# Kernel optimization log

Hardware: AMD Instinct MI355X
Metric: run time of the kernel (lower is better)

Reference implementation:

```python
import jax, jax.numpy as jnp
import numpy as np

B, NPG, DEG, F, H, C = 256, 256, 16, 128, 128, 10
N = B * NPG
E = N * DEG
RATIO = 0.5
K1 = int(np.ceil(RATIO * NPG))       # 128
K2 = int(np.ceil(RATIO * K1))        # 64
K3 = int(np.ceil(RATIO * K2))        # 32


def _glorot(key, shape):
    lim = np.sqrt(6.0 / (shape[0] + shape[1]))
    return jax.random.uniform(key, shape, jnp.float32, -lim, lim)


def setup_inputs() -> dict:
    key = jax.random.key(0)
    ks = jax.random.split(key, 16)
    x = jax.random.normal(ks[0], (N, F), jnp.float32)
    epg = E // B
    g = jnp.repeat(jnp.arange(B, dtype=jnp.int32), epg)
    src = jax.random.randint(ks[1], (E,), 0, NPG, jnp.int32) + g * NPG
    dst = jax.random.randint(ks[2], (E,), 0, NPG, jnp.int32) + g * NPG
    edge_index = jnp.stack([src, dst])
    batch = jnp.repeat(jnp.arange(B, dtype=jnp.int32), NPG)
    return {
        "x": x, "edge_index": edge_index, "batch": batch,
        "W1": _glorot(ks[3], (F, H)), "b1": jnp.zeros((H,), jnp.float32),
        "Wp1": _glorot(ks[4], (H, 1)), "bp1": jnp.zeros((1,), jnp.float32),
        "W2": _glorot(ks[5], (H, H)), "b2": jnp.zeros((H,), jnp.float32),
        "Wp2": _glorot(ks[6], (H, 1)), "bp2": jnp.zeros((1,), jnp.float32),
        "W3": _glorot(ks[7], (H, H)), "b3": jnp.zeros((H,), jnp.float32),
        "Wp3": _glorot(ks[8], (H, 1)), "bp3": jnp.zeros((1,), jnp.float32),
        "Wl1": _glorot(ks[9], (2 * H, H)), "bl1": jnp.zeros((H,), jnp.float32),
        "Wl2": _glorot(ks[10], (H, H // 2)), "bl2": jnp.zeros((H // 2,), jnp.float32),
        "Wl3": _glorot(ks[11], (H // 2, C)), "bl3": jnp.zeros((C,), jnp.float32),
    }


def gcn_conv(x, src, dst, emask, nmask, W, b):
    # PyG GCNConv: symmetric normalization with self-loops, edge weights = emask.
    h = x @ W
    deg = jax.ops.segment_sum(emask, dst, num_segments=N) + nmask  # self-loop on active nodes
    dinv = jnp.where(deg > 0, jax.lax.rsqrt(deg), 0.0)
    w = emask * dinv[src] * dinv[dst]                      # [E]
    agg = jax.ops.segment_sum(h[src] * w[:, None], dst, num_segments=N)
    out = agg + h * (dinv * dinv * nmask)[:, None] + b
    return out * nmask[:, None]


def topk_pool(x, src, dst, emask, nmask, Wp, bp, k):
    # SAGPool-style gcn_pool: score via GCNConv(H->1), per-graph top-k,
    # x <- x * tanh(score) on kept nodes, edges restricted to kept nodes.
    s = gcn_conv(x, src, dst, emask, nmask, Wp, bp)[:, 0]   # [N]
    sm = jnp.where(nmask > 0, s, -jnp.inf).reshape(B, NPG)
    idx = jax.lax.top_k(sm, k)[1]                           # [B,k]
    newmask = jnp.zeros((B, NPG), x.dtype).at[jnp.arange(B)[:, None], idx].set(1.0).reshape(-1)
    x_new = x * jnp.tanh(s)[:, None] * newmask[:, None]
    emask_new = emask * newmask[src] * newmask[dst]
    return x_new, emask_new, newmask


def readout(x, nmask, batch):
    # cat([global_max_pool, global_mean_pool]) over remaining nodes per graph
    cnt = jax.ops.segment_sum(nmask, batch, num_segments=B)
    mean = jax.ops.segment_sum(x, batch, num_segments=B) / cnt[:, None]
    xinf = jnp.where(nmask[:, None] > 0, x, -jnp.inf)
    mx = jax.ops.segment_max(xinf, batch, num_segments=B)
    return jnp.concatenate([mx, mean], axis=1)


def reference(x, edge_index, batch, W1, b1, Wp1, bp1, W2, b2, Wp2, bp2, W3, b3, Wp3, bp3,
              Wl1, bl1, Wl2, bl2, Wl3, bl3):
    src, dst = edge_index[0], edge_index[1]
    emask = jnp.ones((E,), x.dtype)
    nmask = jnp.ones((N,), x.dtype)

    h = jax.nn.relu(gcn_conv(x, src, dst, emask, nmask, W1, b1))
    h, emask, nmask = topk_pool(h, src, dst, emask, nmask, Wp1, bp1, K1)
    x1 = readout(h, nmask, batch)

    h = jax.nn.relu(gcn_conv(h, src, dst, emask, nmask, W2, b2))
    h, emask, nmask = topk_pool(h, src, dst, emask, nmask, Wp2, bp2, K2)
    x2 = readout(h, nmask, batch)

    h = jax.nn.relu(gcn_conv(h, src, dst, emask, nmask, W3, b3))
    h, emask, nmask = topk_pool(h, src, dst, emask, nmask, Wp3, bp3, K3)
    x3 = readout(h, nmask, batch)

    z = x1 + x2 + x3
    z = jax.nn.relu(z @ Wl1 + bl1)   # dropout is identity in eval mode
    z = jax.nn.relu(z @ Wl2 + bl2)
    return jax.nn.log_softmax(z @ Wl3 + bl3, axis=-1)
```

## Files before the change

### kernel.cpp

```cpp
#include <hip/hip_runtime.h>
#include <math.h>

#define NB   256
#define NPG  256
#define NN   (NB * NPG)
#define NE   (NN * 16)
#define EPG  (NE / NB)
#define FD   128
#define NC   10
#define NSL  32
#define NEG_INF (-3.402823466e38f)

struct SM {
    float hs[NPG][FD];
    int   rp[NPG + 4];
    float nmloc[NPG];
    float dvv[NPG];
    float sw[NPG];
    float sf[NPG];
    float svv[NPG];
    float th[NPG];
    float zacc[2 * FD];
    int   si[NPG];
    int   kept[NPG];
    int   anode[NPG];
    float red_mx[16][FD];
    float red_sm[16][FD];
    unsigned char colb[EPG];
};

__device__ __forceinline__ float4& hsq(SM& sm, int v, int q) {
    return *(float4*)&sm.hs[v][(q ^ (v & 7)) << 2];
}

template <int NACT>
__device__ __forceinline__ void do_level(SM& sm,
                                         const float* __restrict__ Wmat,
                                         const float* __restrict__ bias,
                                         const float* __restrict__ Wp,
                                         const float* __restrict__ bpp,
                                         int tid) {
    constexpr int NPS = NACT / NSL;
    constexpr int K   = NACT / 2;
    constexpr int TPN = 1024 / NACT;
    const int f4 = tid & 31;
    const int s  = tid >> 5;

    {
        const int n = tid >> 2, sub = tid & 3;
        float part = 0.f;
        const float nmn = sm.nmloc[n];
        if (nmn > 0.f) {
            const int e1 = sm.rp[n + 1];
            for (int e = sm.rp[n] + sub; e < e1; e += 4)
                part += sm.nmloc[sm.colb[e]];
        }
        part += __shfl_xor(part, 1);
        part += __shfl_xor(part, 2);
        if (sub == 0)
            sm.dvv[n] = (nmn > 0.f) ? rsqrtf(1.f + part) : 0.f;
    }

    {
        int vr[NPS];
        float4 acc[NPS];
#pragma unroll
        for (int c = 0; c < NPS; ++c) {
            vr[c] = sm.anode[c * NSL + s];
            acc[c] = make_float4(0.f, 0.f, 0.f, 0.f);
        }
#pragma unroll 2
        for (int kq = 0; kq < 32; ++kq) {
            const int k0 = kq << 2;
            float4 w0 = *(const float4*)&Wmat[(k0 + 0) * FD + 4 * f4];
            float4 w1 = *(const float4*)&Wmat[(k0 + 1) * FD + 4 * f4];
            float4 w2 = *(const float4*)&Wmat[(k0 + 2) * FD + 4 * f4];
            float4 w3 = *(const float4*)&Wmat[(k0 + 3) * FD + 4 * f4];
#pragma unroll
            for (int c = 0; c < NPS; ++c) {
                float4 hv = hsq(sm, vr[c], kq);
                acc[c].x += hv.x * w0.x + hv.y * w1.x + hv.z * w2.x + hv.w * w3.x;
                acc[c].y += hv.x * w0.y + hv.y * w1.y + hv.z * w2.y + hv.w * w3.y;
                acc[c].z += hv.x * w0.z + hv.y * w1.z + hv.z * w2.z + hv.w * w3.z;
                acc[c].w += hv.x * w0.w + hv.y * w1.w + hv.z * w2.w + hv.w * w3.w;
            }
        }
#pragma unroll
        for (int c = 0; c < NPS; ++c)
            hsq(sm, vr[c], f4) = acc[c];
    }
    __syncthreads();

    const float4 b4  = *(const float4*)&bias[4 * f4];
    const float4 wp4 = *(const float4*)&Wp[4 * f4];
    float4 hreg[NPS];
#pragma unroll
    for (int c = 0; c < NPS; ++c) {
        const int v = sm.anode[c * NSL + s];
        const float dv_ = sm.dvv[v], dv2 = dv_ * dv_;
        const float4 hv = hsq(sm, v, f4);
        float4 acc;
        acc.x = hv.x * dv2 + b4.x;
        acc.y = hv.y * dv2 + b4.y;
        acc.z = hv.z * dv2 + b4.z;
        acc.w = hv.w * dv2 + b4.w;
        const int e0 = sm.rp[v], e1 = sm.rp[v + 1];
        int e = e0;
        for (; e + 4 <= e1; e += 4) {
            int u0 = sm.colb[e],     u1 = sm.colb[e + 1];
            int u2 = sm.colb[e + 2], u3 = sm.colb[e + 3];
            float w0 = sm.dvv[u0] * dv_, w1 = sm.dvv[u1] * dv_;
            float w2 = sm.dvv[u2] * dv_, w3 = sm.dvv[u3] * dv_;
            float4 h0 = hsq(sm, u0, f4);
            float4 h1 = hsq(sm, u1, f4);
            float4 h2 = hsq(sm, u2, f4);
            float4 h3 = hsq(sm, u3, f4);
            acc.x += w0 * h0.x + w1 * h1.x + w2 * h2.x + w3 * h3.x;
            acc.y += w0 * h0.y + w1 * h1.y + w2 * h2.y + w3 * h3.y;
            acc.z += w0 * h0.z + w1 * h1.z + w2 * h2.z + w3 * h3.z;
            acc.w += w0 * h0.w + w1 * h1.w + w2 * h2.w + w3 * h3.w;
        }
        for (; e < e1; ++e) {
            int u = sm.colb[e];
            float w = sm.dvv[u] * dv_;
            float4 hu = hsq(sm, u, f4);
            acc.x += w * hu.x; acc.y += w * hu.y;
            acc.z += w * hu.z; acc.w += w * hu.w;
        }
        acc.x = fmaxf(acc.x, 0.f);
        acc.y = fmaxf(acc.y, 0.f);
        acc.z = fmaxf(acc.z, 0.f);
        acc.w = fmaxf(acc.w, 0.f);
        hreg[c] = acc;
        float p = acc.x * wp4.x + acc.y * wp4.y + acc.z * wp4.z + acc.w * wp4.w;
        p += __shfl_xor(p, 1);
        p += __shfl_xor(p, 2);
        p += __shfl_xor(p, 4);
        p += __shfl_xor(p, 8);
        p += __shfl_xor(p, 16);
        if (f4 == 0) sm.sw[v] = p;
    }
    __syncthreads();

    {
        const int i = tid / TPN, sub = tid % TPN;
        const int v = sm.anode[i];
        const float dv_ = sm.dvv[v];
        float part = 0.f;
        const int e1 = sm.rp[v + 1];
        for (int e = sm.rp[v] + sub; e < e1; e += TPN) {
            int u = sm.colb[e];
            part += sm.dvv[u] * sm.sw[u];
        }
#pragma unroll
        for (int o = 1; o < TPN; o <<= 1) part += __shfl_xor(part, o);
        if (sub == 0) {
            float acc = sm.sw[v] * dv_ * dv_ + bpp[0] + dv_ * part;
            sm.sf[v] = acc;
            sm.svv[i] = acc;
        }
    }
    __syncthreads();

    float v_ = 0.f;
    int   id_ = 0;
    if (tid < NACT) { v_ = sm.svv[tid]; id_ = sm.anode[tid]; }
#pragma unroll
    for (int k = 2; k <= NACT; k <<= 1) {
#pragma unroll
        for (int j = k >> 1; j > 0; j >>= 1) {
            if (j < 64) {
                if (tid < NACT) {
                    float vp = __shfl_xor(v_, j);
                    int  idp = __shfl_xor(id_, j);
                    bool up    = ((tid & k) == 0);
                    bool lower = ((tid & j) == 0);
                    bool g = (v_ > vp) || (v_ == vp && id_ < idp);
                    if (g != (lower == up)) { v_ = vp; id_ = idp; }
                }
            } else {
                if (tid < NACT) { sm.svv[tid] = v_; sm.si[tid] = id_; }
                __syncthreads();
                if (tid < NACT) {
                    int p = tid ^ j;
                    float vp = sm.svv[p];
                    int  idp = sm.si[p];
                    bool up    = ((tid & k) == 0);
                    bool lower = ((tid & j) == 0);
                    bool g = (v_ > vp) || (v_ == vp && id_ < idp);
                    if (g != (lower == up)) { v_ = vp; id_ = idp; }
                }
                __syncthreads();
            }
        }
    }
    if (tid < NPG) sm.kept[tid] = 0;
    __syncthreads();
    if (tid < K) {
        sm.kept[id_] = 1;
        sm.th[id_] = tanhf(sm.sf[id_]);
    }
    __syncthreads();

    float4 mx4 = make_float4(NEG_INF, NEG_INF, NEG_INF, NEG_INF);
    float4 sm4 = make_float4(0.f, 0.f, 0.f, 0.f);
#pragma unroll
    for (int c = 0; c < NPS; ++c) {
        const int v = sm.anode[c * NSL + s];
        if (sm.kept[v]) {
            const float tg = sm.th[v];
            float4 val;
            val.x = hreg[c].x * tg;
            val.y = hreg[c].y * tg;
            val.z = hreg[c].z * tg;
            val.w = hreg[c].w * tg;
            hsq(sm, v, f4) = val;
            mx4.x = fmaxf(mx4.x, val.x); sm4.x += val.x;
            mx4.y = fmaxf(mx4.y, val.y); sm4.y += val.y;
            mx4.z = fmaxf(mx4.z, val.z); sm4.z += val.z;
            mx4.w = fmaxf(mx4.w, val.w); sm4.w += val.w;
        }
    }
    mx4.x = fmaxf(mx4.x, __shfl_xor(mx4.x, 32)); sm4.x += __shfl_xor(sm4.x, 32);
    mx4.y = fmaxf(mx4.y, __shfl_xor(mx4.y, 32)); sm4.y += __shfl_xor(sm4.y, 32);
    mx4.z = fmaxf(mx4.z, __shfl_xor(mx4.z, 32)); sm4.z += __shfl_xor(sm4.z, 32);
    mx4.w = fmaxf(mx4.w, __shfl_xor(mx4.w, 32)); sm4.w += __shfl_xor(sm4.w, 32);
    const int wv = tid >> 6;
    if ((tid & 63) < 32) {
        *(float4*)&sm.red_mx[wv][4 * f4] = mx4;
        *(float4*)&sm.red_sm[wv][4 * f4] = sm4;
    }
    __syncthreads();
    if (tid < FD) {
        float mx = NEG_INF, smv = 0.f;
#pragma unroll
        for (int i = 0; i < 16; ++i) {
            mx = fmaxf(mx, sm.red_mx[i][tid]);
            smv += sm.red_sm[i][tid];
        }
        sm.zacc[tid] += mx;
        sm.zacc[FD + tid] += smv / (float)K;
    }
    if (tid < NPG) sm.nmloc[tid] = (float)sm.kept[tid];
    if (tid < K) sm.anode[tid] = id_;
    __syncthreads();
}

__global__ __launch_bounds__(1024)
void k_mega(const float* __restrict__ x, const int* __restrict__ ei,
            const float* __restrict__ W1, const float* __restrict__ b1,
            const float* __restrict__ Wp1, const float* __restrict__ bp1,
            const float* __restrict__ W2, const float* __restrict__ b2,
            const float* __restrict__ Wp2, const float* __restrict__ bp2,
            const float* __restrict__ W3, const float* __restrict__ b3,
            const float* __restrict__ Wp3, const float* __restrict__ bp3,
            const float* __restrict__ Wl1, const float* __restrict__ bl1,
            const float* __restrict__ Wl2, const float* __restrict__ bl2,
            const float* __restrict__ Wl3, const float* __restrict__ bl3,
            float* __restrict__ out) {
    __shared__ SM sm;
    const int g = blockIdx.x, tid = threadIdx.x;
    const int gbase = g * NPG, ebase = g * EPG;
    const int* __restrict__ srcA = ei;
    const int* __restrict__ dstA = ei + NE;

    int myd[4], mys[4];
#pragma unroll
    for (int i = 0; i < 4; ++i) {
        int e = ebase + tid + i * 1024;
        myd[i] = dstA[e] - gbase;
        mys[i] = srcA[e] - gbase;
    }

    if (tid < NPG) sm.si[tid] = 0;
    __syncthreads();
#pragma unroll
    for (int i = 0; i < 4; ++i) atomicAdd(&sm.si[myd[i]], 1);
    __syncthreads();
    if (tid < NPG) sm.anode[tid] = sm.si[tid];
    __syncthreads();
    for (int o = 1; o < NPG; o <<= 1) {
        int add = 0;
        if (tid < NPG && tid >= o) add = sm.anode[tid - o];
        __syncthreads();
        if (tid < NPG) sm.anode[tid] += add;
        __syncthreads();
    }
    if (tid < NPG) {
        int excl = sm.anode[tid] - sm.si[tid];
        sm.rp[tid] = excl;
        sm.kept[tid] = excl;
        if (tid == 0) sm.rp[NPG] = EPG;
    }
    __syncthreads();
#pragma unroll
    for (int i = 0; i < 4; ++i) {
        int p = atomicAdd(&sm.kept[myd[i]], 1);
        sm.colb[p] = (unsigned char)mys[i];
    }

    {
        const int r0 = tid >> 5, f4 = tid & 31;
        for (int r = r0; r < NPG; r += NSL)
            hsq(sm, r, f4) =
                *(const float4*)&x[((size_t)(gbase + r)) * FD + 4 * f4];
    }
    if (tid < NPG) { sm.anode[tid] = tid; sm.nmloc[tid] = 1.f; }
    if (tid < 2 * FD) sm.zacc[tid] = 0.f;
    __syncthreads();

    do_level<256>(sm, W1, b1, Wp1, bp1, tid);
    do_level<128>(sm, W2, b2, Wp2, bp2, tid);
    do_level<64>(sm, W3, b3, Wp3, bp3, tid);

    if (tid < 128) {
        float a = bl1[tid];
#pragma unroll 8
        for (int k = 0; k < 256; ++k) a += sm.zacc[k] * Wl1[k * 128 + tid];
        sm.sw[tid] = fmaxf(a, 0.f);
    }
    __syncthreads();
    if (tid < 64) {
        float a = bl2[tid];
#pragma unroll 8
        for (int k = 0; k < 128; ++k) a += sm.sw[k] * Wl2[k * 64 + tid];
        sm.sf[tid] = fmaxf(a, 0.f);
    }
    __syncthreads();
    if (tid < NC) {
        float a = bl3[tid];
#pragma unroll
        for (int k = 0; k < 64; ++k) a += sm.sf[k] * Wl3[k * NC + tid];
        sm.svv[tid] = a;
    }
    __syncthreads();
    if (tid == 0) {
        float m = sm.svv[0];
        for (int c = 1; c < NC; ++c) m = fmaxf(m, sm.svv[c]);
        float se = 0.f;
        for (int c = 0; c < NC; ++c) se += expf(sm.svv[c] - m);
        float lse = m + logf(se);
        for (int c = 0; c < NC; ++c) out[g * NC + c] = sm.svv[c] - lse;
    }
}

extern "C" void kernel_launch(void* const* d_in, const int* in_sizes, int n_in,
                              void* d_out, int out_size, void* d_ws, size_t ws_size,
                              hipStream_t stream) {
    const float* x   = (const float*)d_in[0];
    const int*   ei  = (const int*)d_in[1];
    const float* W1  = (const float*)d_in[3];
    const float* b1  = (const float*)d_in[4];
    const float* Wp1 = (const float*)d_in[5];
    const float* bp1 = (const float*)d_in[6];
    const float* W2  = (const float*)d_in[7];
    const float* b2  = (const float*)d_in[8];
    const float* Wp2 = (const float*)d_in[9];
    const float* bp2 = (const float*)d_in[10];
    const float* W3  = (const float*)d_in[11];
    const float* b3  = (const float*)d_in[12];
    const float* Wp3 = (const float*)d_in[13];
    const float* bp3 = (const float*)d_in[14];
    const float* Wl1 = (const float*)d_in[15];
    const float* bl1 = (const float*)d_in[16];
    const float* Wl2 = (const float*)d_in[17];
    const float* bl2 = (const float*)d_in[18];
    const float* Wl3 = (const float*)d_in[19];
    const float* bl3 = (const float*)d_in[20];
    float* out = (float*)d_out;

    k_mega<<<NB, 1024, 0, stream>>>(x, ei,
                                    W1, b1, Wp1, bp1,
                                    W2, b2, Wp2, bp2,
                                    W3, b3, Wp3, bp3,
                                    Wl1, bl1, Wl2, bl2, Wl3, bl3, out);
}
```

Baseline: 127.0 us.

## Fold GCN normalization into the transform, use a wave-level scan, and parallelize the MLP head

Pre-scales each transformed row by its source dinv so aggregation becomes an unweighted sum followed by one multiply by the destination dinv. This removes the per-edge dvv loads and multiplies, and column indices are now read four bytes at a time. Level-one degrees are computed during the CSR build, replacing the log-step shared-memory scan (many barriers) with a wave shuffle scan. The x loads are issued early into registers so they overlap the edge setup. The dense head layers are split across more threads with shuffle reductions. Dropped nodes are written as zeros instead of being skipped.

```diff
diff --git a/kernel.cpp b/kernel.cpp
--- a/kernel.cpp
+++ b/kernel.cpp
@@ -14,7 +14,7 @@
 struct SM {
     float hs[NPG][FD];
     int   rp[NPG + 4];
-    float nmloc[NPG];
+    float nml[NPG];
     float dvv[NPG];
     float sw[NPG];
     float sf[NPG];
@@ -24,6 +24,7 @@
     int   si[NPG];
     int   kept[NPG];
     int   anode[NPG];
+    int   wsum[16];
     float red_mx[16][FD];
     float red_sm[16][FD];
     unsigned char colb[EPG];
@@ -33,7 +34,7 @@
     return *(float4*)&sm.hs[v][(q ^ (v & 7)) << 2];
 }
 
-template <int NACT>
+template <int NACT, bool FIRST>
 __device__ __forceinline__ void do_level(SM& sm,
                                          const float* __restrict__ Wmat,
                                          const float* __restrict__ bias,
@@ -46,19 +47,19 @@
     const int f4 = tid & 31;
     const int s  = tid >> 5;
 
-    {
+    if (!FIRST) {
         const int n = tid >> 2, sub = tid & 3;
         float part = 0.f;
-        const float nmn = sm.nmloc[n];
+        const float nmn = sm.nml[n];
         if (nmn > 0.f) {
             const int e1 = sm.rp[n + 1];
             for (int e = sm.rp[n] + sub; e < e1; e += 4)
-                part += sm.nmloc[sm.colb[e]];
+                part += sm.nml[sm.colb[e]];
         }
         part += __shfl_xor(part, 1);
         part += __shfl_xor(part, 2);
-        if (sub == 0)
-            sm.dvv[n] = (nmn > 0.f) ? rsqrtf(1.f + part) : 0.f;
+        if (sub == 0) sm.dvv[n] = (nmn > 0.f) ? rsqrtf(1.f + part) : 0.f;
+        __syncthreads();
     }
 
     {
@@ -86,8 +87,11 @@
             }
         }
 #pragma unroll
-        for (int c = 0; c < NPS; ++c)
+        for (int c = 0; c < NPS; ++c) {
+            const float d = sm.dvv[vr[c]];
+            acc[c].x *= d; acc[c].y *= d; acc[c].z *= d; acc[c].w *= d;
             hsq(sm, vr[c], f4) = acc[c];
+        }
     }
     __syncthreads();
 
@@ -97,40 +101,38 @@
 #pragma unroll
     for (int c = 0; c < NPS; ++c) {
         const int v = sm.anode[c * NSL + s];
-        const float dv_ = sm.dvv[v], dv2 = dv_ * dv_;
-        const float4 hv = hsq(sm, v, f4);
-        float4 acc;
-        acc.x = hv.x * dv2 + b4.x;
-        acc.y = hv.y * dv2 + b4.y;
-        acc.z = hv.z * dv2 + b4.z;
-        acc.w = hv.w * dv2 + b4.w;
+        const float dv_ = sm.dvv[v];
+        float4 S = hsq(sm, v, f4);
         const int e0 = sm.rp[v], e1 = sm.rp[v + 1];
         int e = e0;
+        int ea = (e0 + 3) & ~3;
+        if (ea > e1) ea = e1;
+        for (; e < ea; ++e) {
+            float4 hu = hsq(sm, sm.colb[e], f4);
+            S.x += hu.x; S.y += hu.y; S.z += hu.z; S.w += hu.w;
+        }
         for (; e + 4 <= e1; e += 4) {
-            int u0 = sm.colb[e],     u1 = sm.colb[e + 1];
-            int u2 = sm.colb[e + 2], u3 = sm.colb[e + 3];
-            float w0 = sm.dvv[u0] * dv_, w1 = sm.dvv[u1] * dv_;
-            float w2 = sm.dvv[u2] * dv_, w3 = sm.dvv[u3] * dv_;
+            unsigned p = *(const unsigned*)&sm.colb[e];
+            int u0 = p & 255, u1 = (p >> 8) & 255;
+            int u2 = (p >> 16) & 255, u3 = p >> 24;
             float4 h0 = hsq(sm, u0, f4);
             float4 h1 = hsq(sm, u1, f4);
             float4 h2 = hsq(sm, u2, f4);
             float4 h3 = hsq(sm, u3, f4);
-            acc.x += w0 * h0.x + w1 * h1.x + w2 * h2.x + w3 * h3.x;
-            acc.y += w0 * h0.y + w1 * h1.y + w2 * h2.y + w3 * h3.y;
-            acc.z += w0 * h0.z + w1 * h1.z + w2 * h2.z + w3 * h3.z;
-            acc.w += w0 * h0.w + w1 * h1.w + w2 * h2.w + w3 * h3.w;
+            S.x += h0.x + h1.x + h2.x + h3.x;
+            S.y += h0.y + h1.y + h2.y + h3.y;
+            S.z += h0.z + h1.z + h2.z + h3.z;
+            S.w += h0.w + h1.w + h2.w + h3.w;
         }
         for (; e < e1; ++e) {
-            int u = sm.colb[e];
-            float w = sm.dvv[u] * dv_;
-            float4 hu = hsq(sm, u, f4);
-            acc.x += w * hu.x; acc.y += w * hu.y;
-            acc.z += w * hu.z; acc.w += w * hu.w;
-        }
-        acc.x = fmaxf(acc.x, 0.f);
-        acc.y = fmaxf(acc.y, 0.f);
-        acc.z = fmaxf(acc.z, 0.f);
-        acc.w = fmaxf(acc.w, 0.f);
+            float4 hu = hsq(sm, sm.colb[e], f4);
+            S.x += hu.x; S.y += hu.y; S.z += hu.z; S.w += hu.w;
+        }
+        float4 acc;
+        acc.x = fmaxf(S.x * dv_ + b4.x, 0.f);
+        acc.y = fmaxf(S.y * dv_ + b4.y, 0.f);
+        acc.z = fmaxf(S.z * dv_ + b4.z, 0.f);
+        acc.w = fmaxf(S.w * dv_ + b4.w, 0.f);
         hreg[c] = acc;
         float p = acc.x * wp4.x + acc.y * wp4.y + acc.z * wp4.z + acc.w * wp4.w;
         p += __shfl_xor(p, 1);
@@ -207,19 +209,21 @@
 #pragma unroll
     for (int c = 0; c < NPS; ++c) {
         const int v = sm.anode[c * NSL + s];
-        if (sm.kept[v]) {
-            const float tg = sm.th[v];
-            float4 val;
-            val.x = hreg[c].x * tg;
-            val.y = hreg[c].y * tg;
-            val.z = hreg[c].z * tg;
-            val.w = hreg[c].w * tg;
-            hsq(sm, v, f4) = val;
-            mx4.x = fmaxf(mx4.x, val.x); sm4.x += val.x;
-            mx4.y = fmaxf(mx4.y, val.y); sm4.y += val.y;
-            mx4.z = fmaxf(mx4.z, val.z); sm4.z += val.z;
-            mx4.w = fmaxf(mx4.w, val.w); sm4.w += val.w;
-        }
+        const int kp = sm.kept[v];
+        const float tg = kp ? sm.th[v] : 0.f;
+        float4 val;
+        val.x = hreg[c].x * tg;
+        val.y = hreg[c].y * tg;
+        val.z = hreg[c].z * tg;
+        val.w = hreg[c].w * tg;
+        hsq(sm, v, f4) = val;
+        if (kp) {
+            mx4.x = fmaxf(mx4.x, val.x);
+            mx4.y = fmaxf(mx4.y, val.y);
+            mx4.z = fmaxf(mx4.z, val.z);
+            mx4.w = fmaxf(mx4.w, val.w);
+        }
+        sm4.x += val.x; sm4.y += val.y; sm4.z += val.z; sm4.w += val.w;
     }
     mx4.x = fmaxf(mx4.x, __shfl_xor(mx4.x, 32)); sm4.x += __shfl_xor(sm4.x, 32);
     mx4.y = fmaxf(mx4.y, __shfl_xor(mx4.y, 32)); sm4.y += __shfl_xor(sm4.y, 32);
@@ -241,8 +245,8 @@
         sm.zacc[tid] += mx;
         sm.zacc[FD + tid] += smv / (float)K;
     }
-    if (tid < NPG) sm.nmloc[tid] = (float)sm.kept[tid];
     if (tid < K) sm.anode[tid] = id_;
+    if (tid < NPG) sm.nml[tid] = (float)sm.kept[tid];
     __syncthreads();
 }
 
@@ -261,36 +265,49 @@
     __shared__ SM sm;
     const int g = blockIdx.x, tid = threadIdx.x;
     const int gbase = g * NPG, ebase = g * EPG;
-    const int* __restrict__ srcA = ei;
-    const int* __restrict__ dstA = ei + NE;
+    const int f4 = tid & 31, s = tid >> 5;
 
     int myd[4], mys[4];
 #pragma unroll
     for (int i = 0; i < 4; ++i) {
         int e = ebase + tid + i * 1024;
-        myd[i] = dstA[e] - gbase;
-        mys[i] = srcA[e] - gbase;
-    }
+        myd[i] = ei[NE + e] - gbase;
+        mys[i] = ei[e] - gbase;
+    }
+    float4 xr[8];
+#pragma unroll
+    for (int c = 0; c < 8; ++c)
+        xr[c] = *(const float4*)&x[((size_t)(gbase + c * NSL + s)) * FD + 4 * f4];
 
     if (tid < NPG) sm.si[tid] = 0;
     __syncthreads();
 #pragma unroll
     for (int i = 0; i < 4; ++i) atomicAdd(&sm.si[myd[i]], 1);
     __syncthreads();
-    if (tid < NPG) sm.anode[tid] = sm.si[tid];
-    __syncthreads();
-    for (int o = 1; o < NPG; o <<= 1) {
-        int add = 0;
-        if (tid < NPG && tid >= o) add = sm.anode[tid - o];
-        __syncthreads();
-        if (tid < NPG) sm.anode[tid] += add;
-        __syncthreads();
-    }
+    int vincl = 0, cnt = 0;
     if (tid < NPG) {
-        int excl = sm.anode[tid] - sm.si[tid];
+        cnt = sm.si[tid];
+        sm.dvv[tid] = rsqrtf(1.f + (float)cnt);
+        vincl = cnt;
+        const int lane = tid & 63;
+#pragma unroll
+        for (int o = 1; o < 64; o <<= 1) {
+            int n = __shfl_up(vincl, o);
+            if (lane >= o) vincl += n;
+        }
+        if (lane == 63) sm.wsum[tid >> 6] = vincl;
+    }
+    __syncthreads();
+    if (tid < NPG) {
+        int base = 0;
+        for (int w = 0; w < (tid >> 6); ++w) base += sm.wsum[w];
+        int excl = base + vincl - cnt;
         sm.rp[tid] = excl;
         sm.kept[tid] = excl;
         if (tid == 0) sm.rp[NPG] = EPG;
+        sm.nml[tid] = 1.f;
+        sm.anode[tid] = tid;
+        sm.zacc[tid] = 0.f;
     }
     __syncthreads();
 #pragma unroll
@@ -298,40 +315,47 @@
         int p = atomicAdd(&sm.kept[myd[i]], 1);
         sm.colb[p] = (unsigned char)mys[i];
     }
+#pragma unroll
+    for (int c = 0; c < 8; ++c)
+        hsq(sm, c * NSL + s, f4) = xr[c];
+    __syncthreads();
+
+    do_level<256, true >(sm, W1, b1, Wp1, bp1, tid);
+    do_level<128, false>(sm, W2, b2, Wp2, bp2, tid);
+    do_level<64,  false>(sm, W3, b3, Wp3, bp3, tid);
 
     {
-        const int r0 = tid >> 5, f4 = tid & 31;
-        for (int r = r0; r < NPG; r += NSL)
-            hsq(sm, r, f4) =
-                *(const float4*)&x[((size_t)(gbase + r)) * FD + 4 * f4];
-    }
-    if (tid < NPG) { sm.anode[tid] = tid; sm.nmloc[tid] = 1.f; }
-    if (tid < 2 * FD) sm.zacc[tid] = 0.f;
-    __syncthreads();
-
-    do_level<256>(sm, W1, b1, Wp1, bp1, tid);
-    do_level<128>(sm, W2, b2, Wp2, bp2, tid);
-    do_level<64>(sm, W3, b3, Wp3, bp3, tid);
-
-    if (tid < 128) {
-        float a = bl1[tid];
-#pragma unroll 8
-        for (int k = 0; k < 256; ++k) a += sm.zacc[k] * Wl1[k * 128 + tid];
-        sm.sw[tid] = fmaxf(a, 0.f);
-    }
-    __syncthreads();
-    if (tid < 64) {
-        float a = bl2[tid];
-#pragma unroll 8
-        for (int k = 0; k < 128; ++k) a += sm.sw[k] * Wl2[k * 64 + tid];
-        sm.sf[tid] = fmaxf(a, 0.f);
-    }
-    __syncthreads();
-    if (tid < NC) {
-        float a = bl3[tid];
-#pragma unroll
-        for (int k = 0; k < 64; ++k) a += sm.sf[k] * Wl3[k * NC + tid];
-        sm.svv[tid] = a;
+        const int o = tid >> 2, sub = tid & 3;
+        if (tid < 512) {
+            float a = 0.f;
+            for (int k = sub; k < 256; k += 4) a += sm.zacc[k] * Wl1[k * 128 + o];
+            a += __shfl_xor(a, 1);
+            a += __shfl_xor(a, 2);
+            if (sub == 0) sm.sw[o] = fmaxf(a + bl1[o], 0.f);
+        }
+    }
+    __syncthreads();
+    {
+        const int o = tid >> 2, sub = tid & 3;
+        if (tid < 256) {
+            float a = 0.f;
+            for (int k = sub; k < 128; k += 4) a += sm.sw[k] * Wl2[k * 64 + o];
+            a += __shfl_xor(a, 1);
+            a += __shfl_xor(a, 2);
+            if (sub == 0) sm.sf[o] = fmaxf(a + bl2[o], 0.f);
+        }
+    }
+    __syncthreads();
+    {
+        const int o = tid >> 3, sub = tid & 7;
+        if (tid < 8 * NC) {
+            float a = 0.f;
+            for (int k = sub; k < 64; k += 8) a += sm.sf[k] * Wl3[k * NC + o];
+            a += __shfl_xor(a, 1);
+            a += __shfl_xor(a, 2);
+            a += __shfl_xor(a, 4);
+            if (sub == 0) sm.svv[o] = a + bl3[o];
+        }
     }
     __syncthreads();
     if (tid == 0) {
```

Result: slower. 143.9 us (+13.3%).
